# Kernel tuning notes

Hardware: AMD Instinct MI355X
Metric: run time of the kernel (lower is better)

The kernel has to match this reference:

```python
import jax, jax.numpy as jnp
import numpy as np

C = 128
PC = 6
NH = 8
HD = C // NH
EPS = 1e-5


def _layernorm(x, g, b):
    m = jnp.mean(x, axis=-1, keepdims=True)
    v = jnp.mean((x - m) ** 2, axis=-1, keepdims=True)
    return (x - m) * jax.lax.rsqrt(v + EPS) * g + b


def setup_inputs() -> dict:
    key = jax.random.key(0)
    ks = jax.random.split(key, 16)
    s = 0.02
    inp = {
        "x": jax.random.normal(ks[0], (2, C, 32, 64, 64), dtype=jnp.float32),
        "polar_coords": jax.random.normal(ks[1], (2, PC, 32, 64, 64), dtype=jnp.float32),
        "Wq": jax.random.normal(ks[2], (C, C), dtype=jnp.float32) * s,
        "bq": jnp.zeros((C,), jnp.float32),
        "Wk": jax.random.normal(ks[3], (C, C), dtype=jnp.float32) * s,
        "bk": jnp.zeros((C,), jnp.float32),
        "Wv": jax.random.normal(ks[4], (C, C), dtype=jnp.float32) * s,
        "bv": jnp.zeros((C,), jnp.float32),
        "Wp": jax.random.normal(ks[5], (PC, C), dtype=jnp.float32) * s,
        "bp": jnp.zeros((C,), jnp.float32),
        "Wo": jax.random.normal(ks[6], (C, C), dtype=jnp.float32) * s,
        "bo": jnp.zeros((C,), jnp.float32),
        "g1": jnp.ones((C,), jnp.float32),
        "beta1": jnp.zeros((C,), jnp.float32),
        "g2": jnp.ones((C,), jnp.float32),
        "beta2": jnp.zeros((C,), jnp.float32),
        "W1": jax.random.normal(ks[7], (C, 4 * C), dtype=jnp.float32) * s,
        "bf1": jnp.zeros((4 * C,), jnp.float32),
        "W2": jax.random.normal(ks[8], (4 * C, C), dtype=jnp.float32) * s,
        "bf2": jnp.zeros((C,), jnp.float32),
    }
    return inp


def reference(x, polar_coords, Wq, bq, Wk, bk, Wv, bv, Wp, bp, Wo, bo,
              g1, beta1, g2, beta2, W1, bf1, W2, bf2):
    B, Cc, D, H, W = x.shape
    N = B * D * H * W
    # [B,C,D,H,W] -> [N,C]
    x_flat = jnp.transpose(x, (0, 2, 3, 4, 1)).reshape(N, Cc)
    polar_flat = jnp.transpose(polar_coords, (0, 2, 3, 4, 1)).reshape(N, -1)

    x_with_polar = x_flat + polar_flat @ Wp + bp
    residual = x_with_polar
    x_norm = _layernorm(x_with_polar, g1, beta1)

    Q = (x_norm @ Wq + bq).reshape(N, NH, HD)
    K = (x_norm @ Wk + bk).reshape(N, NH, HD)
    V = (x_norm @ Wv + bv).reshape(N, NH, HD)

    # tiny per-token cross-head attention: scores [N, NH, NH]
    scores = jnp.einsum('nhd,ngd->nhg', Q, K) / np.float32(np.sqrt(HD))
    attn = jax.nn.softmax(scores, axis=-1)
    attended = jnp.einsum('nhg,ngd->nhd', attn, V).reshape(N, Cc)

    out = attended @ Wo + bo + residual
    residual2 = out
    h = _layernorm(out, g2, beta2)
    h = jax.nn.relu(h @ W1 + bf1) @ W2 + bf2
    out = h + residual2

    out = out.reshape(B, D, H, W, Cc)
    return jnp.transpose(out, (0, 4, 1, 2, 3))
```

## Files before the change

kernel.cpp:

```cpp
#include <hip/hip_runtime.h>

typedef unsigned short u16;
typedef float f32x16 __attribute__((ext_vector_type(16)));
typedef short bf16x8 __attribute__((ext_vector_type(8)));

#define DHW 131072
#define OFF_WQ 0
#define OFF_WK 16384
#define OFF_WV 32768
#define OFF_WO 49152
#define OFF_W1 65536
#define OFF_W2 131072

__device__ __forceinline__ float b2f(u16 u){ union{unsigned i; float f;} x; x.i=((unsigned)u)<<16; return x.f; }
__device__ __forceinline__ u16 f2b(float f){ union{float f; unsigned u;} x; x.f=f; unsigned r=x.u+0x7fffu+((x.u>>16)&1u); return (u16)(r>>16); }
__device__ __forceinline__ unsigned pk2bf(float lo, float hi){
  unsigned r; asm("v_cvt_pk_bf16_f32 %0, %1, %2" : "=v"(r) : "v"(lo), "v"(hi)); return r;
}
__device__ __forceinline__ float lo2f(unsigned u){ union{unsigned i; float f;} x; x.i=u<<16; return x.f; }
__device__ __forceinline__ float hi2f(unsigned u){ union{unsigned i; float f;} x; x.i=u&0xffff0000u; return x.f; }
__device__ __forceinline__ int cofs(int tok, int c){ return (tok<<7) + ((((c>>3) ^ (tok&7)))<<3) + (c&7); }

__global__ void pack_w(const float* __restrict__ Wq, const float* __restrict__ Wk,
                       const float* __restrict__ Wv, const float* __restrict__ Wo,
                       const float* __restrict__ W1, const float* __restrict__ W2,
                       u16* __restrict__ ws){
  int tid = blockIdx.x*256 + threadIdx.x;
  const float* src; int dst, K, N, fb;
  if      (tid <  2048){ src=Wq; dst=OFF_WQ; K=128; N=128; fb=tid;       }
  else if (tid <  4096){ src=Wk; dst=OFF_WK; K=128; N=128; fb=tid-2048;  }
  else if (tid <  6144){ src=Wv; dst=OFF_WV; K=128; N=128; fb=tid-4096;  }
  else if (tid <  8192){ src=Wo; dst=OFF_WO; K=128; N=128; fb=tid-6144;  }
  else if (tid < 16384){ src=W1; dst=OFF_W1; K=128; N=512; fb=tid-8192;  }
  else                 { src=W2; dst=OFF_W2; K=512; N=128; fb=tid-16384; }
  int l = fb & 63, f = fb >> 6;
  int ksc = K >> 4;
  int ct = f / ksc, ks = f - ct*ksc;
  int k0 = ks*16 + ((l>>5)<<3);
  int col = ct*32 + (l&31);
  union { uint4 v; u16 u[8]; } pk;
  #pragma unroll
  for (int j=0;j<8;j++) pk.u[j] = f2b(src[(k0+j)*N + col]);
  *reinterpret_cast<uint4*>(ws + dst + f*512 + l*8) = pk.v;
}

__device__ __forceinline__ f32x16 z16(){ f32x16 z; 
  #pragma unroll
  for(int i=0;i<16;i++) z[i]=0.f; return z; }

__device__ __forceinline__ void mm32(const u16* __restrict__ act, const u16* __restrict__ wf,
                                     int cb, int ksc, int ks0, int tok, int hi, int l,
                                     f32x16 (&acc)[2]){
  #pragma unroll
  for (int kst=0; kst<8; ++kst){
    int g = kst*2 + hi;
    bf16x8 a  = *(const bf16x8*)(act + (tok<<7) + ((g ^ (tok&7))<<3));
    bf16x8 w0 = *(const bf16x8*)(wf + ((cb+0)*ksc + ks0+kst)*512 + l*8);
    bf16x8 w1 = *(const bf16x8*)(wf + ((cb+1)*ksc + ks0+kst)*512 + l*8);
    acc[0] = __builtin_amdgcn_mfma_f32_32x32x16_bf16(w0, a, acc[0], 0,0,0);
    acc[1] = __builtin_amdgcn_mfma_f32_32x32x16_bf16(w1, a, acc[1], 0,0,0);
  }
}
__device__ __forceinline__ void packT32(uint2 (&pk)[2][4], const f32x16 (&acc)[2],
                                        const float* __restrict__ bias, int cbase, int hi, bool relu){
  #pragma unroll
  for (int cw=0;cw<2;cw++)
  #pragma unroll
  for (int q=0;q<4;q++){
    int c0 = cbase + cw*32 + 4*hi + 8*q;
    float v0=acc[cw][q*4+0]+bias[c0],   v1=acc[cw][q*4+1]+bias[c0+1],
          v2=acc[cw][q*4+2]+bias[c0+2], v3=acc[cw][q*4+3]+bias[c0+3];
    if(relu){v0=fmaxf(v0,0.f);v1=fmaxf(v1,0.f);v2=fmaxf(v2,0.f);v3=fmaxf(v3,0.f);}
    pk[cw][q]=(uint2){pk2bf(v0,v1),pk2bf(v2,v3)};
  }
}
__device__ __forceinline__ void store32(u16* dst, const uint2 (&pk)[2][4], int cbase, int tok, int hi){
  #pragma unroll
  for (int cw=0;cw<2;cw++)
  #pragma unroll
  for (int q=0;q<4;q++){
    int c0 = (cbase + cw*32 + 4*hi + 8*q) & 127;
    *(uint2*)&dst[cofs(tok,c0)] = pk[cw][q];
  }
}
__device__ __forceinline__ void load16(const u16* buf, int t, int c0, float* o){
  int g = c0 >> 3;
  union { uint4 v; u16 u[8]; } a, b;
  a.v = *(const uint4*)&buf[(t<<7) + (( g    ^ (t&7))<<3)];
  b.v = *(const uint4*)&buf[(t<<7) + (((g+1) ^ (t&7))<<3)];
  #pragma unroll
  for (int j=0;j<8;j++){ o[j]=b2f(a.u[j]); o[8+j]=b2f(b.u[j]); }
}

__global__ __launch_bounds__(256,3) void fused(
    const float* __restrict__ x, const float* __restrict__ pol,
    const float* __restrict__ Wp, const u16* __restrict__ ws,
    const float* __restrict__ bp, const float* __restrict__ bq,
    const float* __restrict__ bk, const float* __restrict__ bv,
    const float* __restrict__ bo, const float* __restrict__ bf1,
    const float* __restrict__ bf2, const float* __restrict__ g1,
    const float* __restrict__ be1, const float* __restrict__ g2,
    const float* __restrict__ be2, float* __restrict__ out)
{
  __shared__ __align__(16) unsigned char arena[45568];
  u16*   bufA = (u16*)  (arena);
  u16*   bufB = (u16*)  (arena + 16384);
  float* red   = (float*)(arena + 32768);
  float* stats = (float*)(arena + 34816);
  float* parf  = (float*)(arena + 35328);

  const int tid = threadIdx.x;
  const int t   = tid & 63;
  const int p   = __builtin_amdgcn_readfirstlane(tid >> 6);
  const int l   = t;
  const int hi    = l >> 5;
  const int tok   = (p&1)*32 + (l&31);
  const int cbase = (p>>1)*64;
  const int cb2   = (p>>1)*2;

  for (int i=tid; i<2560; i+=256){
    float v;
    if      (i< 128) v = bp [i];
    else if (i< 256) v = g1 [i-128];
    else if (i< 384) v = be1[i-256];
    else if (i< 512) v = g2 [i-384];
    else if (i< 640) v = be2[i-512];
    else if (i<1408) v = Wp [i-640];
    else if (i<1536) v = bq [i-1408];
    else if (i<1664) v = bk [i-1536];
    else if (i<1792) v = bv [i-1664];
    else if (i<1920) v = bo [i-1792];
    else if (i<2048) v = bf2[i-1920];
    else             v = bf1[i-2048];
    parf[i] = v;
  }
  const int bi   = (int)((blockIdx.x*64) >> 17);
  const int dhw0 = (int)((blockIdx.x*64) & (DHW-1));
  const float* xb = x   + (size_t)bi*128*DHW + dhw0;
  const float* pb = pol + (size_t)bi*6*DHW + dhw0;
  float pl6[6];
  #pragma unroll
  for (int j=0;j<6;j++) pl6[j] = pb[(size_t)j*DHW + t];
  __syncthreads();

  float xp[32]; float s1=0.f, s2=0.f;
  #pragma unroll
  for (int it=0; it<32; ++it){
    int c = p*32 + it;
    float a = xb[(size_t)c*DHW + t] + parf[c];
    #pragma unroll
    for (int j=0;j<6;j++) a = fmaf(pl6[j], parf[640 + j*128 + c], a);
    xp[it]=a; s1+=a; s2+=a*a;
  }
  #pragma unroll
  for (int cl=0; cl<4; ++cl){
    uint4 pk = (uint4){ pk2bf(xp[cl*8+0],xp[cl*8+1]), pk2bf(xp[cl*8+2],xp[cl*8+3]),
                        pk2bf(xp[cl*8+4],xp[cl*8+5]), pk2bf(xp[cl*8+6],xp[cl*8+7]) };
    *(uint4*)&bufB[(t<<7) + (((p*4+cl) ^ (t&7))<<3)] = pk;
  }
  red[p*64+t]=s1; red[256+p*64+t]=s2;
  __syncthreads();
  if (tid < 64){
    float a=0.f,b=0.f;
    #pragma unroll
    for (int i=0;i<4;i++){ a+=red[i*64+tid]; b+=red[256+i*64+tid]; }
    float m=a*0.0078125f, v=b*0.0078125f-m*m;
    stats[tid*2]=m; stats[tid*2+1]=rsqrtf(v+1e-5f);
  }
  __syncthreads();

  {
    float mn=stats[t*2], rs=stats[t*2+1];
    #pragma unroll
    for (int cl=0; cl<4; ++cl){
      float y[8];
      #pragma unroll
      for (int j=0;j<8;j++){ int c=p*32+cl*8+j; y[j]=(xp[cl*8+j]-mn)*rs*parf[128+c]+parf[256+c]; }
      uint4 pk = (uint4){ pk2bf(y[0],y[1]), pk2bf(y[2],y[3]), pk2bf(y[4],y[5]), pk2bf(y[6],y[7]) };
      *(uint4*)&bufA[(t<<7) + (((p*4+cl) ^ (t&7))<<3)] = pk;
    }
  }
  uint2 resq[2][4];
  #pragma unroll
  for (int cw=0;cw<2;cw++)
  #pragma unroll
  for (int q=0;q<4;q++){
    int c0 = cbase + cw*32 + 4*hi + 8*q;
    resq[cw][q] = *(const uint2*)&bufB[cofs(tok,c0)];
  }
  __syncthreads();

  uint2 pkt[2][4], pkV[2][4];
  {
    f32x16 acc[2];
    acc[0]=z16(); acc[1]=z16();
    mm32(bufA, ws+OFF_WQ, cb2, 8, 0, tok, hi, l, acc);
    packT32(pkt, acc, parf+1408, cbase, hi, false); store32(bufB, pkt, cbase, tok, hi);
    acc[0]=z16(); acc[1]=z16();
    mm32(bufA, ws+OFF_WV, cb2, 8, 0, tok, hi, l, acc);
    packT32(pkV, acc, parf+1664, cbase, hi, false);
    acc[0]=z16(); acc[1]=z16();
    mm32(bufA, ws+OFF_WK, cb2, 8, 0, tok, hi, l, acc);
    __syncthreads();
    packT32(pkt, acc, parf+1536, cbase, hi, false); store32(bufA, pkt, cbase, tok, hi);
  }
  __syncthreads();

  float sc[16];
  {
    float qv[32];
    load16(bufB, t, p*32, qv); load16(bufB, t, p*32+16, qv+16);
    #pragma unroll
    for (int g8=0; g8<8; ++g8){
      float kv[16]; load16(bufA, t, g8*16, kv);
      float d0=0.f,d1=0.f;
      #pragma unroll
      for (int d=0; d<16; ++d){ d0=fmaf(qv[d],kv[d],d0); d1=fmaf(qv[16+d],kv[d],d1); }
      sc[g8]=d0*0.25f; sc[8+g8]=d1*0.25f;
    }
    #pragma unroll
    for (int hh=0; hh<2; ++hh){
      float mx = sc[hh*8];
      #pragma unroll
      for (int g8=1; g8<8; ++g8) mx = fmaxf(mx, sc[hh*8+g8]);
      float sm=0.f;
      #pragma unroll
      for (int g8=0; g8<8; ++g8){ float e=__expf(sc[hh*8+g8]-mx); sc[hh*8+g8]=e; sm+=e; }
      float inv = 1.f/sm;
      #pragma unroll
      for (int g8=0; g8<8; ++g8) sc[hh*8+g8]*=inv;
    }
  }
  __syncthreads();
  store32(bufA, pkV, cbase, tok, hi);
  __syncthreads();
  {
    float ov[32];
    #pragma unroll
    for (int i=0;i<32;i++) ov[i]=0.f;
    #pragma unroll
    for (int g8=0; g8<8; ++g8){
      float vv[16]; load16(bufA, t, g8*16, vv);
      #pragma unroll
      for (int d=0; d<16; ++d){ ov[d]=fmaf(sc[g8],vv[d],ov[d]); ov[16+d]=fmaf(sc[8+g8],vv[d],ov[16+d]); }
    }
    #pragma unroll
    for (int cl=0; cl<4; ++cl){
      uint4 pk = (uint4){ pk2bf(ov[cl*8+0],ov[cl*8+1]), pk2bf(ov[cl*8+2],ov[cl*8+3]),
                          pk2bf(ov[cl*8+4],ov[cl*8+5]), pk2bf(ov[cl*8+6],ov[cl*8+7]) };
      *(uint4*)&bufB[(t<<7) + (((p*4+cl) ^ (t&7))<<3)] = pk;
    }
  }
  __syncthreads();

  uint2 res2q[2][4];
  {
    f32x16 acc[2];
    acc[0]=z16(); acc[1]=z16();
    mm32(bufB, ws+OFF_WO, cb2, 8, 0, tok, hi, l, acc);
    #pragma unroll
    for (int cw=0;cw<2;cw++)
    #pragma unroll
    for (int q=0;q<4;q++){
      int c0 = cbase + cw*32 + 4*hi + 8*q;
      uint2 r = resq[cw][q];
      float v0 = acc[cw][q*4+0]+parf[1792+c0]  +lo2f(r.x);
      float v1 = acc[cw][q*4+1]+parf[1793+c0]  +hi2f(r.x);
      float v2 = acc[cw][q*4+2]+parf[1794+c0]  +lo2f(r.y);
      float v3 = acc[cw][q*4+3]+parf[1795+c0]  +hi2f(r.y);
      uint2 pk = (uint2){ pk2bf(v0,v1), pk2bf(v2,v3) };
      res2q[cw][q] = pk;
      *(uint2*)&bufA[cofs(tok,c0)] = pk;
    }
  }
  __syncthreads();

  float ovl[32]; s1=0.f; s2=0.f;
  #pragma unroll
  for (int cl=0; cl<4; ++cl){
    union { uint4 v; u16 u[8]; } pk;
    pk.v = *(const uint4*)&bufA[(t<<7) + (((p*4+cl) ^ (t&7))<<3)];
    #pragma unroll
    for (int j=0;j<8;j++){ float v=b2f(pk.u[j]); ovl[cl*8+j]=v; s1+=v; s2+=v*v; }
  }
  red[p*64+t]=s1; red[256+p*64+t]=s2;
  __syncthreads();
  if (tid < 64){
    float a=0.f,b=0.f;
    #pragma unroll
    for (int i=0;i<4;i++){ a+=red[i*64+tid]; b+=red[256+i*64+tid]; }
    float m=a*0.0078125f, v=b*0.0078125f-m*m;
    stats[tid*2]=m; stats[tid*2+1]=rsqrtf(v+1e-5f);
  }
  __syncthreads();
  {
    float mn=stats[t*2], rs=stats[t*2+1];
    #pragma unroll
    for (int cl=0; cl<4; ++cl){
      float y[8];
      #pragma unroll
      for (int j=0;j<8;j++){ int c=p*32+cl*8+j; y[j]=(ovl[cl*8+j]-mn)*rs*parf[384+c]+parf[512+c]; }
      uint4 pk = (uint4){ pk2bf(y[0],y[1]), pk2bf(y[2],y[3]), pk2bf(y[4],y[5]), pk2bf(y[6],y[7]) };
      *(uint4*)&bufB[(t<<7) + (((p*4+cl) ^ (t&7))<<3)] = pk;
    }
  }
  __syncthreads();

  f32x16 acc2[2]; acc2[0]=z16(); acc2[1]=z16();
  #pragma unroll 1
  for (int ch=0; ch<4; ++ch){
    f32x16 acc1[2]; acc1[0]=z16(); acc1[1]=z16();
    mm32(bufB, ws+OFF_W1, ch*4+cb2, 8, 0, tok, hi, l, acc1);
    packT32(pkt, acc1, parf+2048+ch*128, cbase, hi, true); store32(bufA, pkt, cbase, tok, hi);
    __syncthreads();
    mm32(bufA, ws+OFF_W2, cb2, 32, ch*8, tok, hi, l, acc2);
    __syncthreads();
  }

  float* ob = out + (size_t)bi*128*DHW + dhw0;
  #pragma unroll
  for (int cw=0;cw<2;cw++)
  #pragma unroll
  for (int q=0;q<4;q++){
    int c0 = cbase + cw*32 + 4*hi + 8*q;
    uint2 r = res2q[cw][q];
    ob[(size_t)(c0+0)*DHW + tok] = acc2[cw][q*4+0] + parf[1920+c0]   + lo2f(r.x);
    ob[(size_t)(c0+1)*DHW + tok] = acc2[cw][q*4+1] + parf[1921+c0]   + hi2f(r.x);
    ob[(size_t)(c0+2)*DHW + tok] = acc2[cw][q*4+2] + parf[1922+c0]   + lo2f(r.y);
    ob[(size_t)(c0+3)*DHW + tok] = acc2[cw][q*4+3] + parf[1923+c0]   + hi2f(r.y);
  }
}

extern "C" void kernel_launch(void* const* d_in, const int* in_sizes, int n_in,
                              void* d_out, int out_size, void* d_ws, size_t ws_size,
                              hipStream_t stream){
  const float* x   = (const float*)d_in[0];
  const float* pol = (const float*)d_in[1];
  const float* Wq  = (const float*)d_in[2];
  const float* bq  = (const float*)d_in[3];
  const float* Wk  = (const float*)d_in[4];
  const float* bk  = (const float*)d_in[5];
  const float* Wv  = (const float*)d_in[6];
  const float* bv  = (const float*)d_in[7];
  const float* Wp  = (const float*)d_in[8];
  const float* bp  = (const float*)d_in[9];
  const float* Wo  = (const float*)d_in[10];
  const float* bo  = (const float*)d_in[11];
  const float* g1  = (const float*)d_in[12];
  const float* be1 = (const float*)d_in[13];
  const float* g2  = (const float*)d_in[14];
  const float* be2 = (const float*)d_in[15];
  const float* W1  = (const float*)d_in[16];
  const float* bf1 = (const float*)d_in[17];
  const float* W2  = (const float*)d_in[18];
  const float* bf2 = (const float*)d_in[19];
  u16* ws = (u16*)d_ws;
  pack_w<<<96, 256, 0, stream>>>(Wq, Wk, Wv, Wo, W1, W2, ws);
  fused<<<4096, 256, 0, stream>>>(x, pol, Wp, ws, bp, bq, bk, bv, bo, bf1, bf2,
                                  g1, be1, g2, be2, (float*)d_out);
}
```

Measured before the change: 488.2 us.

## Remap MFMA tiling per wave, shrink LDS with bf16 params, raise occupancy

Each wave now owns one 32-column weight tile across both 32-token halves, so it loads one weight fragment per k-step and two activation fragments, where before it loaded two weight fragments and one activation fragment. Parameters are stored in LDS as bf16 rather than fp32, and the layernorm statistics are computed redundantly by every wave instead of through a separate stats pass. Together these drop two barriers, cut LDS per block and raise launch bounds to 4 blocks per SU, aiming for more concurrent blocks and less synchronization. In exchange, biases, gains and Wp are rounded to bf16, which lowers accuracy, and the tighter register budget may cause spills.

```diff
diff --git a/kernel.cpp b/kernel.cpp
--- a/kernel.cpp
+++ b/kernel.cpp
@@ -44,43 +44,48 @@
   *reinterpret_cast<uint4*>(ws + dst + f*512 + l*8) = pk.v;
 }
 
-__device__ __forceinline__ f32x16 z16(){ f32x16 z; 
+__device__ __forceinline__ f32x16 z16(){ f32x16 z;
   #pragma unroll
   for(int i=0;i<16;i++) z[i]=0.f; return z; }
 
 __device__ __forceinline__ void mm32(const u16* __restrict__ act, const u16* __restrict__ wf,
-                                     int cb, int ksc, int ks0, int tok, int hi, int l,
+                                     int ct, int ksc, int ks0, int hi, int l,
                                      f32x16 (&acc)[2]){
+  const int t0 = l & 31, t1 = 32 + (l & 31);
   #pragma unroll
   for (int kst=0; kst<8; ++kst){
+    bf16x8 w  = *(const bf16x8*)(wf + (ct*ksc + ks0+kst)*512 + l*8);
     int g = kst*2 + hi;
-    bf16x8 a  = *(const bf16x8*)(act + (tok<<7) + ((g ^ (tok&7))<<3));
-    bf16x8 w0 = *(const bf16x8*)(wf + ((cb+0)*ksc + ks0+kst)*512 + l*8);
-    bf16x8 w1 = *(const bf16x8*)(wf + ((cb+1)*ksc + ks0+kst)*512 + l*8);
-    acc[0] = __builtin_amdgcn_mfma_f32_32x32x16_bf16(w0, a, acc[0], 0,0,0);
-    acc[1] = __builtin_amdgcn_mfma_f32_32x32x16_bf16(w1, a, acc[1], 0,0,0);
+    bf16x8 a0 = *(const bf16x8*)(act + (t0<<7) + ((g ^ (t0&7))<<3));
+    bf16x8 a1 = *(const bf16x8*)(act + (t1<<7) + ((g ^ (t1&7))<<3));
+    acc[0] = __builtin_amdgcn_mfma_f32_32x32x16_bf16(w, a0, acc[0], 0,0,0);
+    acc[1] = __builtin_amdgcn_mfma_f32_32x32x16_bf16(w, a1, acc[1], 0,0,0);
   }
 }
 __device__ __forceinline__ void packT32(uint2 (&pk)[2][4], const f32x16 (&acc)[2],
-                                        const float* __restrict__ bias, int cbase, int hi, bool relu){
-  #pragma unroll
-  for (int cw=0;cw<2;cw++)
+                                        const u16* __restrict__ bias, int cb, int hi, bool relu){
   #pragma unroll
   for (int q=0;q<4;q++){
-    int c0 = cbase + cw*32 + 4*hi + 8*q;
-    float v0=acc[cw][q*4+0]+bias[c0],   v1=acc[cw][q*4+1]+bias[c0+1],
-          v2=acc[cw][q*4+2]+bias[c0+2], v3=acc[cw][q*4+3]+bias[c0+3];
-    if(relu){v0=fmaxf(v0,0.f);v1=fmaxf(v1,0.f);v2=fmaxf(v2,0.f);v3=fmaxf(v3,0.f);}
-    pk[cw][q]=(uint2){pk2bf(v0,v1),pk2bf(v2,v3)};
-  }
-}
-__device__ __forceinline__ void store32(u16* dst, const uint2 (&pk)[2][4], int cbase, int tok, int hi){
-  #pragma unroll
-  for (int cw=0;cw<2;cw++)
-  #pragma unroll
-  for (int q=0;q<4;q++){
-    int c0 = (cbase + cw*32 + 4*hi + 8*q) & 127;
-    *(uint2*)&dst[cofs(tok,c0)] = pk[cw][q];
+    int c0 = cb + 4*hi + 8*q;
+    float b0=b2f(bias[c0]), b1=b2f(bias[c0+1]), b2v=b2f(bias[c0+2]), b3=b2f(bias[c0+3]);
+    #pragma unroll
+    for (int tt=0;tt<2;tt++){
+      float v0=acc[tt][q*4+0]+b0, v1=acc[tt][q*4+1]+b1,
+            v2=acc[tt][q*4+2]+b2v, v3=acc[tt][q*4+3]+b3;
+      if(relu){v0=fmaxf(v0,0.f);v1=fmaxf(v1,0.f);v2=fmaxf(v2,0.f);v3=fmaxf(v3,0.f);}
+      pk[tt][q]=(uint2){pk2bf(v0,v1),pk2bf(v2,v3)};
+    }
+  }
+}
+__device__ __forceinline__ void store32(u16* dst, const uint2 (&pk)[2][4], int cb, int hi, int l){
+  #pragma unroll
+  for (int tt=0;tt<2;tt++){
+    int tok = tt*32 + (l&31);
+    #pragma unroll
+    for (int q=0;q<4;q++){
+      int c0 = (cb + 4*hi + 8*q) & 127;
+      *(uint2*)&dst[cofs(tok,c0)] = pk[tt][q];
+    }
   }
 }
 __device__ __forceinline__ void load16(const u16* buf, int t, int c0, float* o){
@@ -92,7 +97,7 @@
   for (int j=0;j<8;j++){ o[j]=b2f(a.u[j]); o[8+j]=b2f(b.u[j]); }
 }
 
-__global__ __launch_bounds__(256,3) void fused(
+__global__ __launch_bounds__(256,4) void fused(
     const float* __restrict__ x, const float* __restrict__ pol,
     const float* __restrict__ Wp, const u16* __restrict__ ws,
     const float* __restrict__ bp, const float* __restrict__ bq,
@@ -102,21 +107,18 @@
     const float* __restrict__ be1, const float* __restrict__ g2,
     const float* __restrict__ be2, float* __restrict__ out)
 {
-  __shared__ __align__(16) unsigned char arena[45568];
+  __shared__ __align__(16) unsigned char arena[39936];
   u16*   bufA = (u16*)  (arena);
   u16*   bufB = (u16*)  (arena + 16384);
-  float* red   = (float*)(arena + 32768);
-  float* stats = (float*)(arena + 34816);
-  float* parf  = (float*)(arena + 35328);
+  float* red  = (float*)(arena + 32768);
+  u16*   par  = (u16*)  (arena + 34816);
 
   const int tid = threadIdx.x;
   const int t   = tid & 63;
   const int p   = __builtin_amdgcn_readfirstlane(tid >> 6);
   const int l   = t;
-  const int hi    = l >> 5;
-  const int tok   = (p&1)*32 + (l&31);
-  const int cbase = (p>>1)*64;
-  const int cb2   = (p>>1)*2;
+  const int hi  = l >> 5;
+  const int cb  = p*32;
 
   for (int i=tid; i<2560; i+=256){
     float v;
@@ -132,7 +134,7 @@
     else if (i<1920) v = bo [i-1792];
     else if (i<2048) v = bf2[i-1920];
     else             v = bf1[i-2048];
-    parf[i] = v;
+    par[i] = f2b(v);
   }
   const int bi   = (int)((blockIdx.x*64) >> 17);
   const int dhw0 = (int)((blockIdx.x*64) & (DHW-1));
@@ -147,9 +149,9 @@
   #pragma unroll
   for (int it=0; it<32; ++it){
     int c = p*32 + it;
-    float a = xb[(size_t)c*DHW + t] + parf[c];
-    #pragma unroll
-    for (int j=0;j<6;j++) a = fmaf(pl6[j], parf[640 + j*128 + c], a);
+    float a = xb[(size_t)c*DHW + t] + b2f(par[c]);
+    #pragma unroll
+    for (int j=0;j<6;j++) a = fmaf(pl6[j], b2f(par[640 + j*128 + c]), a);
     xp[it]=a; s1+=a; s2+=a*a;
   }
   #pragma unroll
@@ -160,33 +162,31 @@
   }
   red[p*64+t]=s1; red[256+p*64+t]=s2;
   __syncthreads();
-  if (tid < 64){
+
+  {
     float a=0.f,b=0.f;
     #pragma unroll
-    for (int i=0;i<4;i++){ a+=red[i*64+tid]; b+=red[256+i*64+tid]; }
-    float m=a*0.0078125f, v=b*0.0078125f-m*m;
-    stats[tid*2]=m; stats[tid*2+1]=rsqrtf(v+1e-5f);
-  }
-  __syncthreads();
-
-  {
-    float mn=stats[t*2], rs=stats[t*2+1];
+    for (int i=0;i<4;i++){ a+=red[i*64+t]; b+=red[256+i*64+t]; }
+    float mn=a*0.0078125f, var=b*0.0078125f-mn*mn;
+    float rs=rsqrtf(var+1e-5f);
     #pragma unroll
     for (int cl=0; cl<4; ++cl){
       float y[8];
       #pragma unroll
-      for (int j=0;j<8;j++){ int c=p*32+cl*8+j; y[j]=(xp[cl*8+j]-mn)*rs*parf[128+c]+parf[256+c]; }
+      for (int j=0;j<8;j++){ int c=p*32+cl*8+j; y[j]=(xp[cl*8+j]-mn)*rs*b2f(par[128+c])+b2f(par[256+c]); }
       uint4 pk = (uint4){ pk2bf(y[0],y[1]), pk2bf(y[2],y[3]), pk2bf(y[4],y[5]), pk2bf(y[6],y[7]) };
       *(uint4*)&bufA[(t<<7) + (((p*4+cl) ^ (t&7))<<3)] = pk;
     }
   }
   uint2 resq[2][4];
   #pragma unroll
-  for (int cw=0;cw<2;cw++)
-  #pragma unroll
-  for (int q=0;q<4;q++){
-    int c0 = cbase + cw*32 + 4*hi + 8*q;
-    resq[cw][q] = *(const uint2*)&bufB[cofs(tok,c0)];
+  for (int tt=0;tt<2;tt++){
+    int tok = tt*32 + (l&31);
+    #pragma unroll
+    for (int q=0;q<4;q++){
+      int c0 = cb + 4*hi + 8*q;
+      resq[tt][q] = *(const uint2*)&bufB[cofs(tok,c0)];
+    }
   }
   __syncthreads();
 
@@ -194,15 +194,15 @@
   {
     f32x16 acc[2];
     acc[0]=z16(); acc[1]=z16();
-    mm32(bufA, ws+OFF_WQ, cb2, 8, 0, tok, hi, l, acc);
-    packT32(pkt, acc, parf+1408, cbase, hi, false); store32(bufB, pkt, cbase, tok, hi);
+    mm32(bufA, ws+OFF_WQ, p, 8, 0, hi, l, acc);
+    packT32(pkt, acc, par+1408, cb, hi, false); store32(bufB, pkt, cb, hi, l);
     acc[0]=z16(); acc[1]=z16();
-    mm32(bufA, ws+OFF_WV, cb2, 8, 0, tok, hi, l, acc);
-    packT32(pkV, acc, parf+1664, cbase, hi, false);
+    mm32(bufA, ws+OFF_WV, p, 8, 0, hi, l, acc);
+    packT32(pkV, acc, par+1664, cb, hi, false);
     acc[0]=z16(); acc[1]=z16();
-    mm32(bufA, ws+OFF_WK, cb2, 8, 0, tok, hi, l, acc);
+    mm32(bufA, ws+OFF_WK, p, 8, 0, hi, l, acc);
     __syncthreads();
-    packT32(pkt, acc, parf+1536, cbase, hi, false); store32(bufA, pkt, cbase, tok, hi);
+    packT32(pkt, acc, par+1536, cb, hi, false); store32(bufA, pkt, cb, hi, l);
   }
   __syncthreads();
 
@@ -232,7 +232,7 @@
     }
   }
   __syncthreads();
-  store32(bufA, pkV, cbase, tok, hi);
+  store32(bufA, pkV, cb, hi, l);
   __syncthreads();
   {
     float ov[32];
@@ -257,20 +257,23 @@
   {
     f32x16 acc[2];
     acc[0]=z16(); acc[1]=z16();
-    mm32(bufB, ws+OFF_WO, cb2, 8, 0, tok, hi, l, acc);
-    #pragma unroll
-    for (int cw=0;cw<2;cw++)
+    mm32(bufB, ws+OFF_WO, p, 8, 0, hi, l, acc);
     #pragma unroll
     for (int q=0;q<4;q++){
-      int c0 = cbase + cw*32 + 4*hi + 8*q;
-      uint2 r = resq[cw][q];
-      float v0 = acc[cw][q*4+0]+parf[1792+c0]  +lo2f(r.x);
-      float v1 = acc[cw][q*4+1]+parf[1793+c0]  +hi2f(r.x);
-      float v2 = acc[cw][q*4+2]+parf[1794+c0]  +lo2f(r.y);
-      float v3 = acc[cw][q*4+3]+parf[1795+c0]  +hi2f(r.y);
-      uint2 pk = (uint2){ pk2bf(v0,v1), pk2bf(v2,v3) };
-      res2q[cw][q] = pk;
-      *(uint2*)&bufA[cofs(tok,c0)] = pk;
+      int c0 = cb + 4*hi + 8*q;
+      float b0=b2f(par[1792+c0]), b1=b2f(par[1793+c0]), b2v=b2f(par[1794+c0]), b3=b2f(par[1795+c0]);
+      #pragma unroll
+      for (int tt=0;tt<2;tt++){
+        int tok = tt*32 + (l&31);
+        uint2 r = resq[tt][q];
+        float v0 = acc[tt][q*4+0]+b0+lo2f(r.x);
+        float v1 = acc[tt][q*4+1]+b1+hi2f(r.x);
+        float v2 = acc[tt][q*4+2]+b2v+lo2f(r.y);
+        float v3 = acc[tt][q*4+3]+b3+hi2f(r.y);
+        uint2 pk = (uint2){ pk2bf(v0,v1), pk2bf(v2,v3) };
+        res2q[tt][q] = pk;
+        *(uint2*)&bufA[cofs(tok,c0)] = pk;
+      }
     }
   }
   __syncthreads();
@@ -285,21 +288,17 @@
   }
   red[p*64+t]=s1; red[256+p*64+t]=s2;
   __syncthreads();
-  if (tid < 64){
+  {
     float a=0.f,b=0.f;
     #pragma unroll
-    for (int i=0;i<4;i++){ a+=red[i*64+tid]; b+=red[256+i*64+tid]; }
-    float m=a*0.0078125f, v=b*0.0078125f-m*m;
-    stats[tid*2]=m; stats[tid*2+1]=rsqrtf(v+1e-5f);
-  }
-  __syncthreads();
-  {
-    float mn=stats[t*2], rs=stats[t*2+1];
+    for (int i=0;i<4;i++){ a+=red[i*64+t]; b+=red[256+i*64+t]; }
+    float mn=a*0.0078125f, var=b*0.0078125f-mn*mn;
+    float rs=rsqrtf(var+1e-5f);
     #pragma unroll
     for (int cl=0; cl<4; ++cl){
       float y[8];
       #pragma unroll
-      for (int j=0;j<8;j++){ int c=p*32+cl*8+j; y[j]=(ovl[cl*8+j]-mn)*rs*parf[384+c]+parf[512+c]; }
+      for (int j=0;j<8;j++){ int c=p*32+cl*8+j; y[j]=(ovl[cl*8+j]-mn)*rs*b2f(par[384+c])+b2f(par[512+c]); }
       uint4 pk = (uint4){ pk2bf(y[0],y[1]), pk2bf(y[2],y[3]), pk2bf(y[4],y[5]), pk2bf(y[6],y[7]) };
       *(uint4*)&bufB[(t<<7) + (((p*4+cl) ^ (t&7))<<3)] = pk;
     }
@@ -310,24 +309,27 @@
   #pragma unroll 1
   for (int ch=0; ch<4; ++ch){
     f32x16 acc1[2]; acc1[0]=z16(); acc1[1]=z16();
-    mm32(bufB, ws+OFF_W1, ch*4+cb2, 8, 0, tok, hi, l, acc1);
-    packT32(pkt, acc1, parf+2048+ch*128, cbase, hi, true); store32(bufA, pkt, cbase, tok, hi);
+    mm32(bufB, ws+OFF_W1, ch*4+p, 8, 0, hi, l, acc1);
+    packT32(pkt, acc1, par+2048+ch*128, cb, hi, true); store32(bufA, pkt, cb, hi, l);
     __syncthreads();
-    mm32(bufA, ws+OFF_W2, cb2, 32, ch*8, tok, hi, l, acc2);
-    __syncthreads();
+    mm32(bufA, ws+OFF_W2, p, 32, ch*8, hi, l, acc2);
+    if (ch<3) __syncthreads();
   }
 
   float* ob = out + (size_t)bi*128*DHW + dhw0;
   #pragma unroll
-  for (int cw=0;cw<2;cw++)
-  #pragma unroll
   for (int q=0;q<4;q++){
-    int c0 = cbase + cw*32 + 4*hi + 8*q;
-    uint2 r = res2q[cw][q];
-    ob[(size_t)(c0+0)*DHW + tok] = acc2[cw][q*4+0] + parf[1920+c0]   + lo2f(r.x);
-    ob[(size_t)(c0+1)*DHW + tok] = acc2[cw][q*4+1] + parf[1921+c0]   + hi2f(r.x);
-    ob[(size_t)(c0+2)*DHW + tok] = acc2[cw][q*4+2] + parf[1922+c0]   + lo2f(r.y);
-    ob[(size_t)(c0+3)*DHW + tok] = acc2[cw][q*4+3] + parf[1923+c0]   + hi2f(r.y);
+    int c0 = cb + 4*hi + 8*q;
+    float b0=b2f(par[1920+c0]), b1=b2f(par[1921+c0]), b2v=b2f(par[1922+c0]), b3=b2f(par[1923+c0]);
+    #pragma unroll
+    for (int tt=0;tt<2;tt++){
+      int tok = tt*32 + (l&31);
+      uint2 r = res2q[tt][q];
+      ob[(size_t)(c0+0)*DHW + tok] = acc2[tt][q*4+0] + b0 + lo2f(r.x);
+      ob[(size_t)(c0+1)*DHW + tok] = acc2[tt][q*4+1] + b1 + hi2f(r.x);
+      ob[(size_t)(c0+2)*DHW + tok] = acc2[tt][q*4+2] + b2v + lo2f(r.y);
+      ob[(size_t)(c0+3)*DHW + tok] = acc2[tt][q*4+3] + b3 + hi2f(r.y);
+    }
   }
 }
 
```

New measurement: 555.0 us. 13.7% more time.
